# Kernel optimization log

Measured on AMD Instinct MI355X. Metric: run time of the kernel, lower is better.

## Reference

```python
import jax, jax.numpy as jnp
import numpy as np

B, N, C, H, W = 2, 5, 256, 64, 64
PARA = 256
H0, W0 = 60, 60


def setup_inputs() -> dict:
    key = jax.random.key(0)
    ks = jax.random.split(key, 8)
    s = 0.05
    ys = jnp.linspace(-1.0, 1.0, H0)
    xs = jnp.linspace(-1.0, 1.0, W0)
    gy, gx = jnp.meshgrid(ys, xs, indexing='ij')
    return {
        'feature_map': jax.random.normal(ks[0], (B, C, H, W), jnp.float32),
        'para_code': jax.random.normal(ks[1], (B, PARA), jnp.float32),
        'W1': jax.random.normal(ks[2], (PARA, PARA), jnp.float32) * s,
        'b1': jnp.zeros((PARA,), jnp.float32),
        'Wk': jax.random.normal(ks[3], (2 * N * C, PARA), jnp.float32) * s,
        'bk': jnp.zeros((2 * N * C,), jnp.float32),
        'Ws': jax.random.normal(ks[4], (4 * N * C, PARA), jnp.float32) * s,
        'bs': jnp.zeros((4 * N * C,), jnp.float32),
        'Wr': jax.random.normal(ks[5], (N * C, PARA), jnp.float32) * s,
        'br': jnp.zeros((N * C,), jnp.float32),
        'grid0': jnp.stack([gx, gy], axis=-1),  # (H0, W0, 2), last dim = (x, y)
    }


def _grid_sample_3d(src, grid):
    # src: (B, D, Hs, Ws) single-channel volume; grid: (B, D, Hs, Ws, 3) with (x, y, z)
    # trilinear, zeros padding, align_corners=False (torch F.grid_sample defaults)
    Bn, D, Hn, Wn = src.shape
    x = (grid[..., 0] + 1.0) * (Wn * 0.5) - 0.5
    y = (grid[..., 1] + 1.0) * (Hn * 0.5) - 0.5
    z = (grid[..., 2] + 1.0) * (D * 0.5) - 0.5
    x0f, y0f, z0f = jnp.floor(x), jnp.floor(y), jnp.floor(z)
    tx, ty, tz = x - x0f, y - y0f, z - z0f
    x0, y0, z0 = x0f.astype(jnp.int32), y0f.astype(jnp.int32), z0f.astype(jnp.int32)
    bidx = jnp.arange(Bn)[:, None, None, None]
    out = jnp.zeros_like(x)
    for dz in (0, 1):
        wz = tz if dz else (1.0 - tz)
        zi = z0 + dz
        for dy in (0, 1):
            wy = ty if dy else (1.0 - ty)
            yi = y0 + dy
            for dx in (0, 1):
                wx = tx if dx else (1.0 - tx)
                xi = x0 + dx
                valid = (zi >= 0) & (zi < D) & (yi >= 0) & (yi < Hn) & (xi >= 0) & (xi < Wn)
                v = src[bidx, jnp.clip(zi, 0, D - 1), jnp.clip(yi, 0, Hn - 1), jnp.clip(xi, 0, Wn - 1)]
                out = out + jnp.where(valid, v, 0.0) * (wz * wy * wx)
    return out


def reference(feature_map, para_code, W1, b1, Wk, bk, Ws, bs, Wr, br, grid0):
    Bn, Cn, Hn, Wn = feature_map.shape
    h = jax.nn.relu(para_code @ W1.T + b1)
    kpts = jnp.tanh(h @ Wk.T + bk).reshape(Bn, N, Cn, 2)
    rad = jax.nn.sigmoid(h @ Wr.T + br).reshape(Bn, N, Cn)
    sim = jnp.tanh(h @ Ws.T + bs).reshape(Bn, N, Cn, 4)

    off = grid0[None, None, None] - kpts[:, :, :, None, None, :]   # (B,N,C,H0,W0,2)
    dist = jnp.linalg.norm(off, axis=-1)                           # (B,N,C,H0,W0)
    e = jnp.exp(-dist / rad[:, :, :, None, None])
    scale = (sim[..., 0] + 1.0)[:, :, :, None, None] * e + (1.0 - e)
    ang = (sim[..., 1] * jnp.pi)[:, :, :, None, None] * e
    trans = sim[:, :, :, None, None, 2:] * e[..., None]            # (B,N,C,H0,W0,2)
    c, s_ = jnp.cos(ang), jnp.sin(ang)
    # offset @ R^T with R = [[cos, sin], [-sin, cos]]
    rx = off[..., 0] * c + off[..., 1] * s_
    ry = -off[..., 0] * s_ + off[..., 1] * c
    rot = jnp.stack([rx, ry], axis=-1)
    warped = scale[..., None] * rot + trans + kpts[:, :, :, None, None, :]
    wts = jax.nn.softmax(e, axis=1)                                # softmax over keypoints N
    g2 = jnp.sum(warped * wts[..., None], axis=1)                  # (B,C,H0,W0,2)

    # faithful reproduction of the transpose/permute/contiguous-view scramble in the torch code
    g2 = jnp.swapaxes(g2, -1, -2)                                  # (B,C,H0,2,W0)
    g2 = jnp.transpose(g2, (0, 1, 4, 2, 3))                        # (B,C,W0,H0,2)
    g2 = g2.reshape(Bn, Cn * 2, H0, W0)
    # torchvision Resize applied twice in the source; the second (H,W)->(H,W) bilinear resize is identity
    g2 = jax.image.resize(g2, (Bn, Cn * 2, Hn, Wn), 'bilinear')
    g2 = g2.reshape(Bn, Cn, 2, Hn, Wn).transpose(0, 1, 3, 4, 2)    # (B,C,H,W,2)

    depth = jnp.linspace(-1.0 + 1.0 / Cn, 1.0 - 1.0 / Cn, Cn)
    depth = jnp.broadcast_to(depth[None, :, None, None, None], (Bn, Cn, Hn, Wn, 1))
    grid3 = jnp.concatenate([g2, depth], axis=-1)                  # (B,C,H,W,3)
    return _grid_sample_3d(feature_map, grid3)                     # (B,C,H,W)
```

## Files before the change

### kernel.cpp

```cpp
#include <hip/hip_runtime.h>
#include <math.h>

#define B_ 2
#define N_ 5
#define C_ 256
#define H_ 64
#define W_ 64
#define PARA_ 256
#define H0_ 60
#define W0_ 60
#define LOG2E 1.4426950408889634f

__global__ void k_mlp1(const float* __restrict__ pc, const float* __restrict__ W1,
                       const float* __restrict__ b1, float* __restrict__ h) {
    int b = blockIdx.x;
    int j = threadIdx.x;
    __shared__ float spc[PARA_];
    spc[j] = pc[b * PARA_ + j];
    __syncthreads();
    const float* wrow = W1 + (size_t)j * PARA_;
    float acc = b1[j];
    #pragma unroll 8
    for (int k = 0; k < PARA_; ++k) acc += spc[k] * wrow[k];
    h[b * PARA_ + j] = fmaxf(acc, 0.f);
}

__global__ void k_heads(const float* __restrict__ h,
                        const float* __restrict__ Wk, const float* __restrict__ bk,
                        const float* __restrict__ Ws, const float* __restrict__ bs,
                        const float* __restrict__ Wr, const float* __restrict__ br,
                        float* __restrict__ kpts, float* __restrict__ rad,
                        float* __restrict__ sim) {
    int b = blockIdx.x / 35;
    int m = (blockIdx.x % 35) * 256 + threadIdx.x;
    __shared__ float sh[PARA_];
    sh[threadIdx.x] = h[b * PARA_ + threadIdx.x];
    __syncthreads();

    const float* wrow;
    float bias;
    int kind, j;
    if (m < 2 * N_ * C_) {
        j = m; wrow = Wk + (size_t)j * PARA_; bias = bk[j]; kind = 0;
    } else if (m < 3 * N_ * C_) {
        j = m - 2 * N_ * C_; wrow = Wr + (size_t)j * PARA_; bias = br[j]; kind = 1;
    } else {
        j = m - 3 * N_ * C_; wrow = Ws + (size_t)j * PARA_; bias = bs[j]; kind = 2;
    }
    float acc = bias;
    #pragma unroll 8
    for (int k = 0; k < PARA_; ++k) acc += sh[k] * wrow[k];

    if (kind == 0)      kpts[b * 2 * N_ * C_ + j] = tanhf(acc);
    else if (kind == 1) rad [b * N_ * C_     + j] = 1.f / (1.f + expf(-acc));
    else                sim [b * 4 * N_ * C_ + j] = tanhf(acc);
}

__global__ __launch_bounds__(256) void k_warp(const float* __restrict__ kpts,
                       const float* __restrict__ rad,
                       const float* __restrict__ sim,
                       const float* __restrict__ grid0,
                       float* __restrict__ scram) {
    int blk  = blockIdx.x;
    int half = blk & 1;
    int bc   = blk >> 1;
    int c = bc % C_;
    int b = bc / C_;

    float kx[N_], ky[N_], nlr[N_], s0_[N_], s1h[N_], s2_[N_], s3_[N_];
    #pragma unroll
    for (int n = 0; n < N_; ++n) {
        int base = (b * N_ + n) * C_ + c;
        kx[n]  = kpts[base * 2 + 0];
        ky[n]  = kpts[base * 2 + 1];
        nlr[n] = -LOG2E * __builtin_amdgcn_rcpf(rad[base]);
        s0_[n] = sim[base * 4 + 0];
        s1h[n] = sim[base * 4 + 1] * 0.5f;
        s2_[n] = sim[base * 4 + 2];
        s3_[n] = sim[base * 4 + 3];
    }

    float* plane = scram + ((size_t)(b * 2 * C_ + 2 * c)) * 3600;

    int qend = half * 1800 + 1800;
    for (int q = half * 1800 + threadIdx.x; q < qend; q += 256) {
        int h0 = q % 60, w0 = q / 60;
        float2 g = *(const float2*)(grid0 + (h0 * W0_ + w0) * 2);
        float gx = g.x, gy = g.y;

        float numx = 0.f, numy = 0.f, den = 0.f;
        #pragma unroll
        for (int n = 0; n < N_; ++n) {
            float ox = gx - kx[n], oy = gy - ky[n];
            float dist = __builtin_amdgcn_sqrtf(fmaf(ox, ox, oy * oy));
            float e = __builtin_amdgcn_exp2f(dist * nlr[n]);
            float scale = fmaf(s0_[n], e, 1.f);
            float ar = s1h[n] * e;
            float sn = __builtin_amdgcn_sinf(ar);
            float cs = __builtin_amdgcn_cosf(ar);
            float rx = fmaf(ox, cs, oy * sn);
            float ry = fmaf(oy, cs, -(ox * sn));
            float wxv = fmaf(scale, rx, fmaf(s2_[n], e, kx[n]));
            float wyv = fmaf(scale, ry, fmaf(s3_[n], e, ky[n]));
            float sw = __builtin_amdgcn_exp2f(e * LOG2E);
            numx = fmaf(wxv, sw, numx);
            numy = fmaf(wyv, sw, numy);
            den += sw;
        }
        float inv = __builtin_amdgcn_rcpf(den);
        float2 outv = make_float2(numx * inv, numy * inv);
        *(float2*)(plane + w0 * 120 + h0 * 2) = outv;
    }
}

__global__ __launch_bounds__(256) void k_sample(const float* __restrict__ scram,
                         const float* __restrict__ fmap,
                         float* __restrict__ out) {
    int idx = blockIdx.x * 256 + threadIdx.x;
    int w = idx % W_;
    int tmp = idx / W_;
    int h = tmp % H_; tmp /= H_;
    int c = tmp % C_;
    int b = tmp / C_;

    const float sc = 60.f / 64.f;
    float chf = ((float)h + 0.5f) * sc - 0.5f;
    float cwf = ((float)w + 0.5f) * sc - 0.5f;
    int ih = (int)floorf(chf), iw = (int)floorf(cwf);
    float th = chf - (float)ih, tw = cwf - (float)iw;
    int ih0 = min(max(ih, 0), H0_ - 1), ih1 = min(max(ih + 1, 0), H0_ - 1);
    int iw0 = min(max(iw, 0), W0_ - 1), iw1 = min(max(iw + 1, 0), W0_ - 1);
    float w00 = (1.f - th) * (1.f - tw), w01 = (1.f - th) * tw;
    float w10 = th * (1.f - tw),         w11 = th * tw;

    float g[2];
    #pragma unroll
    for (int t = 0; t < 2; ++t) {
        const float* chp = scram + ((size_t)(b * 2 * C_ + 2 * c + t)) * (H0_ * W0_);
        g[t] = w00 * chp[ih0 * W0_ + iw0] + w01 * chp[ih0 * W0_ + iw1]
             + w10 * chp[ih1 * W0_ + iw0] + w11 * chp[ih1 * W0_ + iw1];
    }

    float x = (g[0] + 1.f) * ((float)W_ * 0.5f) - 0.5f;
    float y = (g[1] + 1.f) * ((float)H_ * 0.5f) - 0.5f;
    int x0 = (int)floorf(x), y0 = (int)floorf(y);
    float tx = x - (float)x0, ty = y - (float)y0;
    const float* fm = fmap + ((size_t)(b * C_ + c)) * (H_ * W_);
    float acc = 0.f;
    #pragma unroll
    for (int dy = 0; dy < 2; ++dy) {
        int yi = y0 + dy;
        float wy = dy ? ty : (1.f - ty);
        if (yi < 0 || yi >= H_) continue;
        #pragma unroll
        for (int dx = 0; dx < 2; ++dx) {
            int xi = x0 + dx;
            float wx = dx ? tx : (1.f - tx);
            if (xi < 0 || xi >= W_) continue;
            acc += fm[yi * W_ + xi] * wy * wx;
        }
    }
    out[idx] = acc;
}

extern "C" void kernel_launch(void* const* d_in, const int* in_sizes, int n_in,
                              void* d_out, int out_size, void* d_ws, size_t ws_size,
                              hipStream_t stream) {
    const float* fmap  = (const float*)d_in[0];
    const float* pc    = (const float*)d_in[1];
    const float* W1    = (const float*)d_in[2];
    const float* b1    = (const float*)d_in[3];
    const float* Wk    = (const float*)d_in[4];
    const float* bk    = (const float*)d_in[5];
    const float* Ws    = (const float*)d_in[6];
    const float* bs    = (const float*)d_in[7];
    const float* Wr    = (const float*)d_in[8];
    const float* br    = (const float*)d_in[9];
    const float* grid0 = (const float*)d_in[10];

    float* ws = (float*)d_ws;
    float* h     = ws;
    float* kpts  = ws + 512;
    float* rad   = ws + 5632;
    float* sim   = ws + 8192;
    float* scram = ws + 18432;

    k_mlp1 <<<B_, 256, 0, stream>>>(pc, W1, b1, h);
    k_heads<<<B_ * 35, 256, 0, stream>>>(h, Wk, bk, Ws, bs, Wr, br, kpts, rad, sim);
    k_warp <<<B_ * C_ * 2, 256, 0, stream>>>(kpts, rad, sim, grid0, scram);
    k_sample<<<(B_ * C_ * H_ * W_) / 256, 256, 0, stream>>>(scram, fmap, (float*)d_out);
}
```

Baseline: 130.6 us.

## Fuse warp and sample kernels via shared memory; fold MLP1 into heads

The per-channel warp-grid computation and the bilinear/trilinear sampling are merged into one kernel per (b,c). The scrambled grid plane and the feature map slice are held in LDS, which removes the global scratch round trip and one launch. The first MLP layer is recomputed inside each heads block, dropping another launch, and the dot products now use float4 loads. In exchange each block uses about 45KB of LDS with 512 threads, which may limit occupancy, and W1 is recomputed redundantly across 35 blocks per batch.

```diff
diff --git a/kernel.cpp b/kernel.cpp
--- a/kernel.cpp
+++ b/kernel.cpp
@@ -11,30 +11,35 @@
 #define W0_ 60
 #define LOG2E 1.4426950408889634f
 
-__global__ void k_mlp1(const float* __restrict__ pc, const float* __restrict__ W1,
-                       const float* __restrict__ b1, float* __restrict__ h) {
-    int b = blockIdx.x;
-    int j = threadIdx.x;
-    __shared__ float spc[PARA_];
-    spc[j] = pc[b * PARA_ + j];
-    __syncthreads();
-    const float* wrow = W1 + (size_t)j * PARA_;
-    float acc = b1[j];
-    #pragma unroll 8
-    for (int k = 0; k < PARA_; ++k) acc += spc[k] * wrow[k];
-    h[b * PARA_ + j] = fmaxf(acc, 0.f);
-}
-
-__global__ void k_heads(const float* __restrict__ h,
-                        const float* __restrict__ Wk, const float* __restrict__ bk,
-                        const float* __restrict__ Ws, const float* __restrict__ bs,
-                        const float* __restrict__ Wr, const float* __restrict__ br,
-                        float* __restrict__ kpts, float* __restrict__ rad,
-                        float* __restrict__ sim) {
+__global__ __launch_bounds__(256) void k_heads(
+        const float* __restrict__ pc, const float* __restrict__ W1,
+        const float* __restrict__ b1,
+        const float* __restrict__ Wk, const float* __restrict__ bk,
+        const float* __restrict__ Ws, const float* __restrict__ bs,
+        const float* __restrict__ Wr, const float* __restrict__ br,
+        float* __restrict__ kpts, float* __restrict__ rad,
+        float* __restrict__ sim) {
     int b = blockIdx.x / 35;
     int m = (blockIdx.x % 35) * 256 + threadIdx.x;
+    int tid = threadIdx.x;
+
+    __shared__ float spc[PARA_];
     __shared__ float sh[PARA_];
-    sh[threadIdx.x] = h[b * PARA_ + threadIdx.x];
+    spc[tid] = pc[b * PARA_ + tid];
+    __syncthreads();
+
+    {
+        const float4* wrow = (const float4*)(W1 + (size_t)tid * PARA_);
+        const float4* sp4 = (const float4*)spc;
+        float acc = b1[tid];
+        #pragma unroll 8
+        for (int k = 0; k < PARA_ / 4; ++k) {
+            float4 wv = wrow[k];
+            float4 pv = sp4[k];
+            acc += wv.x * pv.x + wv.y * pv.y + wv.z * pv.z + wv.w * pv.w;
+        }
+        sh[tid] = fmaxf(acc, 0.f);
+    }
     __syncthreads();
 
     const float* wrow;
@@ -47,25 +52,38 @@
     } else {
         j = m - 3 * N_ * C_; wrow = Ws + (size_t)j * PARA_; bias = bs[j]; kind = 2;
     }
+    const float4* w4 = (const float4*)wrow;
+    const float4* h4 = (const float4*)sh;
     float acc = bias;
     #pragma unroll 8
-    for (int k = 0; k < PARA_; ++k) acc += sh[k] * wrow[k];
+    for (int k = 0; k < PARA_ / 4; ++k) {
+        float4 wv = w4[k];
+        float4 hv = h4[k];
+        acc += wv.x * hv.x + wv.y * hv.y + wv.z * hv.z + wv.w * hv.w;
+    }
 
     if (kind == 0)      kpts[b * 2 * N_ * C_ + j] = tanhf(acc);
     else if (kind == 1) rad [b * N_ * C_     + j] = 1.f / (1.f + expf(-acc));
     else                sim [b * 4 * N_ * C_ + j] = tanhf(acc);
 }
 
-__global__ __launch_bounds__(256) void k_warp(const float* __restrict__ kpts,
-                       const float* __restrict__ rad,
-                       const float* __restrict__ sim,
-                       const float* __restrict__ grid0,
-                       float* __restrict__ scram) {
-    int blk  = blockIdx.x;
-    int half = blk & 1;
-    int bc   = blk >> 1;
-    int c = bc % C_;
-    int b = bc / C_;
+__global__ __launch_bounds__(512) void k_fused(
+        const float* __restrict__ kpts, const float* __restrict__ rad,
+        const float* __restrict__ sim, const float* __restrict__ grid0,
+        const float* __restrict__ fmap, float* __restrict__ out) {
+    int c = blockIdx.x & (C_ - 1);
+    int b = blockIdx.x >> 8;
+    int tid = threadIdx.x;
+
+    __shared__ __align__(16) float sg[7200];
+    __shared__ __align__(16) float sf[H_ * W_];
+
+    {
+        const float4* fp = (const float4*)(fmap + ((size_t)(b * C_ + c)) * (H_ * W_));
+        float4* sf4 = (float4*)sf;
+        sf4[tid]       = fp[tid];
+        sf4[tid + 512] = fp[tid + 512];
+    }
 
     float kx[N_], ky[N_], nlr[N_], s0_[N_], s1h[N_], s2_[N_], s3_[N_];
     #pragma unroll
@@ -80,10 +98,7 @@
         s3_[n] = sim[base * 4 + 3];
     }
 
-    float* plane = scram + ((size_t)(b * 2 * C_ + 2 * c)) * 3600;
-
-    int qend = half * 1800 + 1800;
-    for (int q = half * 1800 + threadIdx.x; q < qend; q += 256) {
+    for (int q = tid; q < H0_ * W0_; q += 512) {
         int h0 = q % 60, w0 = q / 60;
         float2 g = *(const float2*)(grid0 + (h0 * W0_ + w0) * 2);
         float gx = g.x, gy = g.y;
@@ -108,59 +123,50 @@
             den += sw;
         }
         float inv = __builtin_amdgcn_rcpf(den);
-        float2 outv = make_float2(numx * inv, numy * inv);
-        *(float2*)(plane + w0 * 120 + h0 * 2) = outv;
+        *(float2*)(sg + w0 * 120 + h0 * 2) = make_float2(numx * inv, numy * inv);
     }
-}
+    __syncthreads();
 
-__global__ __launch_bounds__(256) void k_sample(const float* __restrict__ scram,
-                         const float* __restrict__ fmap,
-                         float* __restrict__ out) {
-    int idx = blockIdx.x * 256 + threadIdx.x;
-    int w = idx % W_;
-    int tmp = idx / W_;
-    int h = tmp % H_; tmp /= H_;
-    int c = tmp % C_;
-    int b = tmp / C_;
+    float* outp = out + ((size_t)(b * C_ + c)) * (H_ * W_);
+    for (int p = tid; p < H_ * W_; p += 512) {
+        int w = p & (W_ - 1);
+        int h = p >> 6;
 
-    const float sc = 60.f / 64.f;
-    float chf = ((float)h + 0.5f) * sc - 0.5f;
-    float cwf = ((float)w + 0.5f) * sc - 0.5f;
-    int ih = (int)floorf(chf), iw = (int)floorf(cwf);
-    float th = chf - (float)ih, tw = cwf - (float)iw;
-    int ih0 = min(max(ih, 0), H0_ - 1), ih1 = min(max(ih + 1, 0), H0_ - 1);
-    int iw0 = min(max(iw, 0), W0_ - 1), iw1 = min(max(iw + 1, 0), W0_ - 1);
-    float w00 = (1.f - th) * (1.f - tw), w01 = (1.f - th) * tw;
-    float w10 = th * (1.f - tw),         w11 = th * tw;
+        const float sc = 60.f / 64.f;
+        float chf = ((float)h + 0.5f) * sc - 0.5f;
+        float cwf = ((float)w + 0.5f) * sc - 0.5f;
+        int ih = (int)floorf(chf), iw = (int)floorf(cwf);
+        float th = chf - (float)ih, tw = cwf - (float)iw;
+        int ih0 = min(max(ih, 0), H0_ - 1), ih1 = min(max(ih + 1, 0), H0_ - 1);
+        int iw0 = min(max(iw, 0), W0_ - 1), iw1 = min(max(iw + 1, 0), W0_ - 1);
+        float w00 = (1.f - th) * (1.f - tw), w01 = (1.f - th) * tw;
+        float w10 = th * (1.f - tw),         w11 = th * tw;
 
-    float g[2];
-    #pragma unroll
-    for (int t = 0; t < 2; ++t) {
-        const float* chp = scram + ((size_t)(b * 2 * C_ + 2 * c + t)) * (H0_ * W0_);
-        g[t] = w00 * chp[ih0 * W0_ + iw0] + w01 * chp[ih0 * W0_ + iw1]
-             + w10 * chp[ih1 * W0_ + iw0] + w11 * chp[ih1 * W0_ + iw1];
+        float g0 = w00 * sg[ih0 * 60 + iw0] + w01 * sg[ih0 * 60 + iw1]
+                 + w10 * sg[ih1 * 60 + iw0] + w11 * sg[ih1 * 60 + iw1];
+        float g1 = w00 * sg[3600 + ih0 * 60 + iw0] + w01 * sg[3600 + ih0 * 60 + iw1]
+                 + w10 * sg[3600 + ih1 * 60 + iw0] + w11 * sg[3600 + ih1 * 60 + iw1];
+
+        float x = (g0 + 1.f) * ((float)W_ * 0.5f) - 0.5f;
+        float y = (g1 + 1.f) * ((float)H_ * 0.5f) - 0.5f;
+        int x0 = (int)floorf(x), y0 = (int)floorf(y);
+        float tx = x - (float)x0, ty = y - (float)y0;
+        float acc = 0.f;
+        #pragma unroll
+        for (int dy = 0; dy < 2; ++dy) {
+            int yi = y0 + dy;
+            float wy = dy ? ty : (1.f - ty);
+            if (yi < 0 || yi >= H_) continue;
+            #pragma unroll
+            for (int dx = 0; dx < 2; ++dx) {
+                int xi = x0 + dx;
+                float wx = dx ? tx : (1.f - tx);
+                if (xi < 0 || xi >= W_) continue;
+                acc += sf[yi * W_ + xi] * wy * wx;
+            }
+        }
+        outp[p] = acc;
     }
-
-    float x = (g[0] + 1.f) * ((float)W_ * 0.5f) - 0.5f;
-    float y = (g[1] + 1.f) * ((float)H_ * 0.5f) - 0.5f;
-    int x0 = (int)floorf(x), y0 = (int)floorf(y);
-    float tx = x - (float)x0, ty = y - (float)y0;
-    const float* fm = fmap + ((size_t)(b * C_ + c)) * (H_ * W_);
-    float acc = 0.f;
-    #pragma unroll
-    for (int dy = 0; dy < 2; ++dy) {
-        int yi = y0 + dy;
-        float wy = dy ? ty : (1.f - ty);
-        if (yi < 0 || yi >= H_) continue;
-        #pragma unroll
-        for (int dx = 0; dx < 2; ++dx) {
-            int xi = x0 + dx;
-            float wx = dx ? tx : (1.f - tx);
-            if (xi < 0 || xi >= W_) continue;
-            acc += fm[yi * W_ + xi] * wy * wx;
-        }
-    }
-    out[idx] = acc;
 }
 
 extern "C" void kernel_launch(void* const* d_in, const int* in_sizes, int n_in,
@@ -179,14 +185,11 @@
     const float* grid0 = (const float*)d_in[10];
 
     float* ws = (float*)d_ws;
-    float* h     = ws;
-    float* kpts  = ws + 512;
-    float* rad   = ws + 5632;
-    float* sim   = ws + 8192;
-    float* scram = ws + 18432;
+    float* kpts = ws;
+    float* rad  = ws + 5120;
+    float* sim  = ws + 7680;
 
-    k_mlp1 <<<B_, 256, 0, stream>>>(pc, W1, b1, h);
-    k_heads<<<B_ * 35, 256, 0, stream>>>(h, Wk, bk, Ws, bs, Wr, br, kpts, rad, sim);
-    k_warp <<<B_ * C_ * 2, 256, 0, stream>>>(kpts, rad, sim, grid0, scram);
-    k_sample<<<(B_ * C_ * H_ * W_) / 256, 256, 0, stream>>>(scram, fmap, (float*)d_out);
+    k_heads<<<B_ * 35, 256, 0, stream>>>(pc, W1, b1, Wk, bk, Ws, bs, Wr, br,
+                                         kpts, rad, sim);
+    k_fused<<<B_ * C_, 512, 0, stream>>>(kpts, rad, sim, grid0, fmap, (float*)d_out);
 }
```

After: 116.3 us. -10.9%, faster.
